# Kernel optimization log

Measured on AMD Instinct MI355X. Metric: run time of the kernel, lower is better.

The kernel has to match this reference:

```python
import jax, jax.numpy as jnp
import numpy as np

B, S, D, E, K = 4, 2048, 1024, 8, 2
EPS, W_THRES, TEMP = 1e-4, 0.1, 1.0


def setup_inputs() -> dict:
    key = jax.random.key(0)
    k1, k2, k3, k4, k5 = jax.random.split(key, 5)
    x = jax.random.normal(k1, (B, S, D), dtype=jnp.float32)
    gate_W = jax.random.normal(k2, (D, E), dtype=jnp.float32) * 0.02
    gate_b = jnp.zeros((E,), dtype=jnp.float32)
    expert_W = jax.random.normal(k3, (E, D, D), dtype=jnp.float32) * 0.02
    expert_b = jnp.zeros((E, D), dtype=jnp.float32)
    return {"x": x, "gate_W": gate_W, "gate_b": gate_b,
            "expert_W": expert_W, "expert_b": expert_b}


def reference(x, gate_W, gate_b, expert_W, expert_b):
    # Gating: linear -> temperature -> clamp-min(eps) -> softmax
    scores = jnp.maximum((x @ gate_W + gate_b) / TEMP, EPS)      # [B,S,E]
    p = jax.nn.softmax(scores, axis=-1)                           # [B,S,E]
    _, topk_idx = jax.lax.top_k(p, K)                             # [B,S,K]
    # boolean membership mask of selected experts
    topk_mask = jax.nn.one_hot(topk_idx, E, dtype=p.dtype).sum(-2) > 0  # [B,S,E]
    # weights: clamp-min(weight_thres), normalized by detached sum over selected
    w = jnp.maximum(p, W_THRES)                                   # [B,S,E]
    w_gather = jnp.take_along_axis(w, topk_idx, axis=-1)          # [B,S,K]
    total = jax.lax.stop_gradient(w_gather.sum(-1, keepdims=True))
    w = w / total
    comb = jnp.where(topk_mask, w, jnp.zeros_like(w))             # [B,S,E]
    # Dense equivalent of gather/expert/scatter loop (E small): each expert
    # is Linear(D, D); masked combine weights zero out unselected experts.
    y = jnp.einsum('bsd,edf->bsef', x, expert_W) + expert_b       # [B,S,E,D]
    out = jnp.einsum('bsef,bse->bsf', y, comb) / K                # [B,S,D]
    return out
```

## Files before the change

kernel.cpp:

```cpp
#include <hip/hip_runtime.h>
#include <stdint.h>

#define TOK 8192
#define DIM 1024
#define NE 8
#define NTILE 136

typedef short bf16x8 __attribute__((ext_vector_type(8)));
typedef float f32x4 __attribute__((ext_vector_type(4)));

__device__ __forceinline__ unsigned short f2bf(float f) {
  unsigned int u = __float_as_uint(f);
  u += 0x7FFFu + ((u >> 16) & 1u);
  return (unsigned short)(u >> 16);
}

__device__ __forceinline__ void gl_lds16(const void* g, void* l) {
  __builtin_amdgcn_global_load_lds(
      (__attribute__((address_space(1))) unsigned int*)(g),
      (__attribute__((address_space(3))) unsigned int*)(l), 16, 0, 0);
}

__global__ void zero_cnt(int* cnt) {
  if (threadIdx.x < NE) cnt[threadIdx.x] = 0;
}

__global__ __launch_bounds__(256) void gate_kernel(
    const float* __restrict__ x, const float* __restrict__ gW,
    const float* __restrict__ gb, unsigned short* __restrict__ xb,
    int* __restrict__ eSel, float* __restrict__ wSel)
{
  const int wave = threadIdx.x >> 6;
  const int lane = threadIdx.x & 63;
  const int t = blockIdx.x * 4 + wave;
  const float4* xrow = (const float4*)(x + (size_t)t * DIM);
  ushort4* xbrow = (ushort4*)(xb + (size_t)t * DIM);

  double acc[NE];
#pragma unroll
  for (int e = 0; e < NE; ++e) acc[e] = 0.0;

#pragma unroll
  for (int i = 0; i < 4; ++i) {
    const int j = i * 64 + lane;
    float4 v = xrow[j];
    ushort4 pk;
    pk.x = f2bf(v.x); pk.y = f2bf(v.y); pk.z = f2bf(v.z); pk.w = f2bf(v.w);
    xbrow[j] = pk;
    const float* g = gW + (size_t)j * 4 * NE;
    float xv[4] = {v.x, v.y, v.z, v.w};
#pragma unroll
    for (int c = 0; c < 4; ++c) {
#pragma unroll
      for (int e = 0; e < NE; ++e)
        acc[e] += (double)xv[c] * (double)g[c * NE + e];
    }
  }
#pragma unroll
  for (int off = 32; off > 0; off >>= 1) {
#pragma unroll
    for (int e = 0; e < NE; ++e)
      acc[e] += __shfl_xor(acc[e], off, 64);
  }

  if (lane == 0) {
    double s[NE];
#pragma unroll
    for (int e = 0; e < NE; ++e) {
      s[e] = acc[e] + (double)gb[e];
      if (s[e] < 1e-4) s[e] = 1e-4;
    }
    int e0 = 0;
    for (int e = 1; e < NE; ++e) if (s[e] > s[e0]) e0 = e;
    int e1 = (e0 == 0) ? 1 : 0;
    for (int e = 0; e < NE; ++e) if (e != e0 && s[e] > s[e1]) e1 = e;
    float m = (float)s[e0];
    float Z = 0.f, pf[NE];
#pragma unroll
    for (int e = 0; e < NE; ++e) { pf[e] = __expf((float)s[e] - m); Z += pf[e]; }
    float w0 = pf[e0] / Z; if (w0 < 0.1f) w0 = 0.1f;
    float w1 = pf[e1] / Z; if (w1 < 0.1f) w1 = 0.1f;
    const float inv = 0.5f / (w0 + w1);
    eSel[t * 2 + 0] = e0;
    eSel[t * 2 + 1] = e1;
    wSel[t * 2 + 0] = w0 * inv;
    wSel[t * 2 + 1] = w1 * inv;
  }
}

__global__ __launch_bounds__(256) void scatter_kernel(
    const int* __restrict__ eSel, const float* __restrict__ wSel,
    int* __restrict__ cnt, int* __restrict__ listTok, float* __restrict__ listW)
{
  __shared__ int lcnt[NE];
  __shared__ int base[NE];
  const int tid = threadIdx.x;
  if (tid < NE) lcnt[tid] = 0;
  __syncthreads();

  const int t = blockIdx.x * 256 + tid;
  const int e0 = eSel[t * 2 + 0];
  const int e1 = eSel[t * 2 + 1];
  const float w0 = wSel[t * 2 + 0];
  const float w1 = wSel[t * 2 + 1];
  const int l0 = atomicAdd(&lcnt[e0], 1);
  const int l1 = atomicAdd(&lcnt[e1], 1);
  __syncthreads();
  if (tid < NE) base[tid] = atomicAdd(&cnt[tid], lcnt[tid]);
  __syncthreads();

  const int p0 = base[e0] + l0;
  listTok[e0 * TOK + p0] = t * 2 + 0;
  listW [e0 * TOK + p0] = w0;
  const int p1 = base[e1] + l1;
  listTok[e1 * TOK + p1] = t * 2 + 1;
  listW [e1 * TOK + p1] = w1;
}

__global__ __launch_bounds__(256) void transpose_w(
    const float* __restrict__ W, unsigned short* __restrict__ Wt)
{
  __shared__ float tile[32][33];
  const int e = blockIdx.z;
  const int d0 = blockIdx.y * 32, f0 = blockIdx.x * 32;
  const int tx = threadIdx.x & 31, ty = threadIdx.x >> 5;
  const float* src = W + ((size_t)e * DIM + d0) * DIM + f0;
#pragma unroll
  for (int r = ty; r < 32; r += 8)
    tile[r][tx] = src[(size_t)r * DIM + tx];
  __syncthreads();
  unsigned short* dst = Wt + ((size_t)e * DIM + f0) * DIM + d0;
#pragma unroll
  for (int r = ty; r < 32; r += 8)
    dst[(size_t)r * DIM + tx] = f2bf(tile[tx][r]);
}

__global__ void build_desc(const int* __restrict__ cnt, int* __restrict__ tiles)
{
  if (threadIdx.x == 0 && blockIdx.x == 0) {
    int n = 0;
    for (int e = 0; e < NE; ++e) {
      int c = cnt[e];
      for (int r = 0; r < c; r += 128) {
        tiles[1 + n * 3] = e;
        tiles[2 + n * 3] = r;
        tiles[3 + n * 3] = (c - r < 128) ? (c - r) : 128;
        ++n;
      }
    }
    tiles[0] = n;
  }
}

__global__ __launch_bounds__(256) void moe_gemm(
    const unsigned short* __restrict__ xb, const unsigned short* __restrict__ Wt,
    const float* __restrict__ eb, const int* __restrict__ tiles,
    const int* __restrict__ listTok, const float* __restrict__ listW,
    float* __restrict__ yslot)
{
  const int dId = blockIdx.x % NTILE;
  const int cT  = blockIdx.x / NTILE;
  if (dId >= tiles[0]) return;
  const int e    = tiles[1 + dId * 3];
  const int r0   = tiles[2 + dId * 3];
  const int rows = tiles[3 + dId * 3];

  __shared__ __align__(16) unsigned short As[2][128 * 32];
  __shared__ __align__(16) unsigned short Bs[2][128 * 32];
  __shared__ int   tid_s[128];
  __shared__ float w_s[128];

  const int tid = threadIdx.x;
  if (tid < 128) {
    if (tid < rows) {
      tid_s[tid] = listTok[e * TOK + r0 + tid];
      w_s[tid]   = listW [e * TOK + r0 + tid];
    } else {
      tid_s[tid] = 0;
      w_s[tid]   = 0.0f;
    }
  }
  __syncthreads();

  const int w    = tid >> 6;
  const int lane = tid & 63;
  const int qsrc = (lane & 3) ^ ((lane >> 3) & 3);
  const int rA0  = w * 32 + (lane >> 2);
  const int rA1  = rA0 + 16;
  const unsigned short* srcA0 = xb + (size_t)(tid_s[rA0] >> 1) * DIM + qsrc * 8;
  const unsigned short* srcA1 = xb + (size_t)(tid_s[rA1] >> 1) * DIM + qsrc * 8;
  const unsigned short* srcB0 = Wt + ((size_t)e * DIM + cT * 128 + rA0) * DIM + qsrc * 8;
  const unsigned short* srcB1 = Wt + ((size_t)e * DIM + cT * 128 + rA1) * DIM + qsrc * 8;

  const int wr = w >> 1, wc = w & 1;
  const int mrow = lane & 15;
  const int qg   = lane >> 4;
  const int qsA  = (qg ^ ((mrow >> 1) & 3)) * 8;

  f32x4 acc[4][4];
#pragma unroll
  for (int i = 0; i < 4; ++i)
#pragma unroll
    for (int j = 0; j < 4; ++j)
      acc[i][j] = {0.f, 0.f, 0.f, 0.f};

  gl_lds16(srcA0, &As[0][w * 1024]);
  gl_lds16(srcA1, &As[0][w * 1024 + 512]);
  gl_lds16(srcB0, &Bs[0][w * 1024]);
  gl_lds16(srcB1, &Bs[0][w * 1024 + 512]);

#pragma unroll 2
  for (int kc = 0; kc < DIM / 32; ++kc) {
    const int cur = kc & 1;
    __syncthreads();
    if (kc < DIM / 32 - 1) {
      const int k1 = (kc + 1) * 32;
      unsigned short* a = &As[cur ^ 1][w * 1024];
      unsigned short* b = &Bs[cur ^ 1][w * 1024];
      gl_lds16(srcA0 + k1, a);
      gl_lds16(srcA1 + k1, a + 512);
      gl_lds16(srcB0 + k1, b);
      gl_lds16(srcB1 + k1, b + 512);
    }
    bf16x8 af[4], bfr[4];
#pragma unroll
    for (int mt = 0; mt < 4; ++mt)
      af[mt] = *(const bf16x8*)&As[cur][(wr * 64 + mt * 16 + mrow) * 32 + qsA];
#pragma unroll
    for (int nt = 0; nt < 4; ++nt)
      bfr[nt] = *(const bf16x8*)&Bs[cur][(wc * 64 + nt * 16 + mrow) * 32 + qsA];
#pragma unroll
    for (int mt = 0; mt < 4; ++mt)
#pragma unroll
      for (int nt = 0; nt < 4; ++nt)
        acc[mt][nt] = __builtin_amdgcn_mfma_f32_16x16x32_bf16(
            af[mt], bfr[nt], acc[mt][nt], 0, 0, 0);
  }

  const int colBase = cT * 128 + wc * 64 + mrow;
  float bias[4];
#pragma unroll
  for (int nt = 0; nt < 4; ++nt)
    bias[nt] = eb[(size_t)e * DIM + colBase + nt * 16];
#pragma unroll
  for (int mt = 0; mt < 4; ++mt) {
#pragma unroll
    for (int r = 0; r < 4; ++r) {
      const int rloc = wr * 64 + mt * 16 + (lane >> 4) * 4 + r;
      if (rloc < rows) {
        const int tk    = tid_s[rloc];
        const float wgt = w_s[rloc];
        float* dst = yslot + ((size_t)(tk & 1) * TOK + (size_t)(tk >> 1)) * DIM;
#pragma unroll
        for (int nt = 0; nt < 4; ++nt)
          dst[colBase + nt * 16] = wgt * (acc[mt][nt][r] + bias[nt]);
      }
    }
  }
}

__global__ __launch_bounds__(256) void combine(
    const float4* __restrict__ y0, const float4* __restrict__ y1,
    float4* __restrict__ out)
{
  const size_t i = (size_t)blockIdx.x * 256 + threadIdx.x;
  float4 a = y0[i], b = y1[i];
  float4 o;
  o.x = a.x + b.x; o.y = a.y + b.y; o.z = a.z + b.z; o.w = a.w + b.w;
  out[i] = o;
}

extern "C" void kernel_launch(void* const* d_in, const int* in_sizes, int n_in,
                              void* d_out, int out_size, void* d_ws, size_t ws_size,
                              hipStream_t stream)
{
  const float* x  = (const float*)d_in[0];
  const float* gW = (const float*)d_in[1];
  const float* gb = (const float*)d_in[2];
  const float* eW = (const float*)d_in[3];
  const float* eb = (const float*)d_in[4];
  float* out = (float*)d_out;

  char* p = (char*)d_ws;
  unsigned short* xb = (unsigned short*)p;  p += (size_t)TOK * DIM * 2;
  unsigned short* Wt = (unsigned short*)p;  p += (size_t)NE * DIM * DIM * 2;
  float* yslot = (float*)p;                 p += (size_t)2 * TOK * DIM * 4;
  int* cnt = (int*)p;                       p += 256;
  int* listTok = (int*)p;                   p += (size_t)NE * TOK * 4;
  float* listW = (float*)p;                 p += (size_t)NE * TOK * 4;
  int* tiles = (int*)p;                     p += 4096;

  int*   eSel = (int*)yslot;
  float* wSel = (float*)(yslot + TOK * 2);

  zero_cnt<<<1, 64, 0, stream>>>(cnt);
  gate_kernel<<<TOK / 4, 256, 0, stream>>>(x, gW, gb, xb, eSel, wSel);
  scatter_kernel<<<TOK / 256, 256, 0, stream>>>(eSel, wSel, cnt, listTok, listW);
  transpose_w<<<dim3(32, 32, 8), 256, 0, stream>>>(eW, Wt);
  build_desc<<<1, 64, 0, stream>>>(cnt, tiles);
  moe_gemm<<<NTILE * 8, 256, 0, stream>>>(xb, Wt, eb, tiles, listTok, listW, yslot);
  combine<<<TOK * DIM / 4 / 256, 256, 0, stream>>>(
      (const float4*)yslot, (const float4*)yslot + (size_t)TOK * DIM / 4, (float4*)out);
}
```

Before: 237.3 us.

## Pre-tile expert weights into MFMA fragment layout and load B from global directly

The weight transpose kernel now writes bf16 weights in a fragment-ordered layout, so each lane's B operand is one contiguous 16-byte global load. This removes the B tiles from LDS and their async copies. The zero_cnt and build_desc launches are also folded away: the gate kernel zeroes the counters, and each GEMM block derives its tile from the expert counts. B loads now come straight from global/L2 each k-step with no LDS reuse across waves, which adds latency and memory traffic. The transpose kernel now has only 512 blocks, each running a serial loop over K.

```diff
diff --git a/kernel.cpp b/kernel.cpp
--- a/kernel.cpp
+++ b/kernel.cpp
@@ -21,15 +21,13 @@
       (__attribute__((address_space(3))) unsigned int*)(l), 16, 0, 0);
 }
 
-__global__ void zero_cnt(int* cnt) {
-  if (threadIdx.x < NE) cnt[threadIdx.x] = 0;
-}
-
 __global__ __launch_bounds__(256) void gate_kernel(
     const float* __restrict__ x, const float* __restrict__ gW,
     const float* __restrict__ gb, unsigned short* __restrict__ xb,
-    int* __restrict__ eSel, float* __restrict__ wSel)
-{
+    int* __restrict__ eSel, float* __restrict__ wSel, int* __restrict__ cnt)
+{
+  if (blockIdx.x == 0 && threadIdx.x < NE) cnt[threadIdx.x] = 0;
+
   const int wave = threadIdx.x >> 6;
   const int lane = threadIdx.x & 63;
   const int t = blockIdx.x * 4 + wave;
@@ -120,53 +118,53 @@
 __global__ __launch_bounds__(256) void transpose_w(
     const float* __restrict__ W, unsigned short* __restrict__ Wt)
 {
-  __shared__ float tile[32][33];
-  const int e = blockIdx.z;
-  const int d0 = blockIdx.y * 32, f0 = blockIdx.x * 32;
-  const int tx = threadIdx.x & 31, ty = threadIdx.x >> 5;
-  const float* src = W + ((size_t)e * DIM + d0) * DIM + f0;
-#pragma unroll
-  for (int r = ty; r < 32; r += 8)
-    tile[r][tx] = src[(size_t)r * DIM + tx];
-  __syncthreads();
-  unsigned short* dst = Wt + ((size_t)e * DIM + f0) * DIM + d0;
-#pragma unroll
-  for (int r = ty; r < 32; r += 8)
-    dst[(size_t)r * DIM + tx] = f2bf(tile[tx][r]);
-}
-
-__global__ void build_desc(const int* __restrict__ cnt, int* __restrict__ tiles)
-{
-  if (threadIdx.x == 0 && blockIdx.x == 0) {
-    int n = 0;
-    for (int e = 0; e < NE; ++e) {
-      int c = cnt[e];
-      for (int r = 0; r < c; r += 128) {
-        tiles[1 + n * 3] = e;
-        tiles[2 + n * 3] = r;
-        tiles[3 + n * 3] = (c - r < 128) ? (c - r) : 128;
-        ++n;
-      }
-    }
-    tiles[0] = n;
+  __shared__ float t[32 * 17 + 16];
+  const int e  = blockIdx.x >> 6;
+  const int fb = blockIdx.x & 63;
+  const int f0 = fb * 16;
+  const int tid = threadIdx.x;
+  const float* Wb = W + (size_t)e * DIM * DIM + f0;
+  unsigned short* Ob = Wt + ((size_t)(e * 64 + fb) * 32) * 512;
+
+  for (int kc = 0; kc < 32; ++kc) {
+    const int d0 = kc * 32;
+    __syncthreads();
+#pragma unroll
+    for (int h = 0; h < 512; h += 256) {
+      const int idx = tid + h;
+      t[(idx >> 4) * 17 + (idx & 15)] = Wb[(size_t)(d0 + (idx >> 4)) * DIM + (idx & 15)];
+    }
+    __syncthreads();
+#pragma unroll
+    for (int h = 0; h < 512; h += 256) {
+      const int o = tid + h;
+      Ob[(size_t)kc * 512 + o] = f2bf(t[(o & 31) * 17 + (o >> 5)]);
+    }
   }
 }
 
 __global__ __launch_bounds__(256) void moe_gemm(
     const unsigned short* __restrict__ xb, const unsigned short* __restrict__ Wt,
-    const float* __restrict__ eb, const int* __restrict__ tiles,
+    const float* __restrict__ eb, const int* __restrict__ cnt,
     const int* __restrict__ listTok, const float* __restrict__ listW,
     float* __restrict__ yslot)
 {
   const int dId = blockIdx.x % NTILE;
   const int cT  = blockIdx.x / NTILE;
-  if (dId >= tiles[0]) return;
-  const int e    = tiles[1 + dId * 3];
-  const int r0   = tiles[2 + dId * 3];
-  const int rows = tiles[3 + dId * 3];
+  int e = -1, r0 = 0, rows = 0, accT = 0;
+#pragma unroll
+  for (int ee = 0; ee < NE; ++ee) {
+    const int c = cnt[ee];
+    const int nt = (c + 127) >> 7;
+    if (dId >= accT && dId < accT + nt) {
+      e = ee; r0 = (dId - accT) * 128;
+      rows = c - r0; if (rows > 128) rows = 128;
+    }
+    accT += nt;
+  }
+  if (e < 0) return;
 
   __shared__ __align__(16) unsigned short As[2][128 * 32];
-  __shared__ __align__(16) unsigned short Bs[2][128 * 32];
   __shared__ int   tid_s[128];
   __shared__ float w_s[128];
 
@@ -189,14 +187,15 @@
   const int rA1  = rA0 + 16;
   const unsigned short* srcA0 = xb + (size_t)(tid_s[rA0] >> 1) * DIM + qsrc * 8;
   const unsigned short* srcA1 = xb + (size_t)(tid_s[rA1] >> 1) * DIM + qsrc * 8;
-  const unsigned short* srcB0 = Wt + ((size_t)e * DIM + cT * 128 + rA0) * DIM + qsrc * 8;
-  const unsigned short* srcB1 = Wt + ((size_t)e * DIM + cT * 128 + rA1) * DIM + qsrc * 8;
 
   const int wr = w >> 1, wc = w & 1;
   const int mrow = lane & 15;
   const int qg   = lane >> 4;
   const int qsA  = (qg ^ ((mrow >> 1) & 3)) * 8;
 
+  const unsigned short* bbase =
+      Wt + ((size_t)(e * 64 + cT * 8 + wc * 4) * 32) * 512 + mrow * 32 + qg * 8;
+
   f32x4 acc[4][4];
 #pragma unroll
   for (int i = 0; i < 4; ++i)
@@ -206,35 +205,30 @@
 
   gl_lds16(srcA0, &As[0][w * 1024]);
   gl_lds16(srcA1, &As[0][w * 1024 + 512]);
-  gl_lds16(srcB0, &Bs[0][w * 1024]);
-  gl_lds16(srcB1, &Bs[0][w * 1024 + 512]);
-
-#pragma unroll 2
+
   for (int kc = 0; kc < DIM / 32; ++kc) {
     const int cur = kc & 1;
     __syncthreads();
+    bf16x8 b[4];
+#pragma unroll
+    for (int nt = 0; nt < 4; ++nt)
+      b[nt] = *(const bf16x8*)(bbase + (size_t)nt * 16384 + kc * 512);
     if (kc < DIM / 32 - 1) {
       const int k1 = (kc + 1) * 32;
       unsigned short* a = &As[cur ^ 1][w * 1024];
-      unsigned short* b = &Bs[cur ^ 1][w * 1024];
       gl_lds16(srcA0 + k1, a);
       gl_lds16(srcA1 + k1, a + 512);
-      gl_lds16(srcB0 + k1, b);
-      gl_lds16(srcB1 + k1, b + 512);
-    }
-    bf16x8 af[4], bfr[4];
+    }
+    bf16x8 af[4];
 #pragma unroll
     for (int mt = 0; mt < 4; ++mt)
       af[mt] = *(const bf16x8*)&As[cur][(wr * 64 + mt * 16 + mrow) * 32 + qsA];
 #pragma unroll
     for (int nt = 0; nt < 4; ++nt)
-      bfr[nt] = *(const bf16x8*)&Bs[cur][(wc * 64 + nt * 16 + mrow) * 32 + qsA];
-#pragma unroll
-    for (int mt = 0; mt < 4; ++mt)
-#pragma unroll
-      for (int nt = 0; nt < 4; ++nt)
+#pragma unroll
+      for (int mt = 0; mt < 4; ++mt)
         acc[mt][nt] = __builtin_amdgcn_mfma_f32_16x16x32_bf16(
-            af[mt], bfr[nt], acc[mt][nt], 0, 0, 0);
+            af[mt], b[nt], acc[mt][nt], 0, 0, 0);
   }
 
   const int colBase = cT * 128 + wc * 64 + mrow;
@@ -288,17 +282,14 @@
   int* cnt = (int*)p;                       p += 256;
   int* listTok = (int*)p;                   p += (size_t)NE * TOK * 4;
   float* listW = (float*)p;                 p += (size_t)NE * TOK * 4;
-  int* tiles = (int*)p;                     p += 4096;
 
   int*   eSel = (int*)yslot;
   float* wSel = (float*)(yslot + TOK * 2);
 
-  zero_cnt<<<1, 64, 0, stream>>>(cnt);
-  gate_kernel<<<TOK / 4, 256, 0, stream>>>(x, gW, gb, xb, eSel, wSel);
+  gate_kernel<<<TOK / 4, 256, 0, stream>>>(x, gW, gb, xb, eSel, wSel, cnt);
   scatter_kernel<<<TOK / 256, 256, 0, stream>>>(eSel, wSel, cnt, listTok, listW);
-  transpose_w<<<dim3(32, 32, 8), 256, 0, stream>>>(eW, Wt);
-  build_desc<<<1, 64, 0, stream>>>(cnt, tiles);
-  moe_gemm<<<NTILE * 8, 256, 0, stream>>>(xb, Wt, eb, tiles, listTok, listW, yslot);
+  transpose_w<<<NE * 64, 256, 0, stream>>>(eW, Wt);
+  moe_gemm<<<NTILE * 8, 256, 0, stream>>>(xb, Wt, eb, cnt, listTok, listW, yslot);
   combine<<<TOK * DIM / 4 / 256, 256, 0, stream>>>(
       (const float4*)yslot, (const float4*)yslot + (size_t)TOK * DIM / 4, (float4*)out);
 }
```

Result: no change. 233.2 us (-1.7%).
